# Performance work log

Measured on AMD Instinct MI355X. Metric: run time of the kernel, lower is better.

## Reference

```python
import jax, jax.numpy as jnp
import numpy as np

EPS = 1e-5
KS = 3
PAD = 1


def _bn(x, g, b, m, v):
    inv = g / jnp.sqrt(v + EPS)
    return x * inv[None, :, None, None] + (b - m * inv)[None, :, None, None]


def _deform_conv2d(x, off_w, off_b, w):
    # x: (B,C,H,W); off_w: (2*9,C,3,3); w: (Cout,C,3,3)
    B, C, H, W = x.shape
    N = KS * KS
    off = jax.lax.conv_general_dilated(x, off_w, (1, 1), ((PAD, PAD), (PAD, PAD)))
    off = off + off_b[None, :, None, None]                      # (B,2N,H,W)
    xp = jnp.pad(x, ((0, 0), (0, 0), (PAD, PAD), (PAD, PAD)))
    Hp, Wp = H + 2 * PAD, W + 2 * PAD
    r = jnp.arange(KS, dtype=x.dtype) - (KS - 1) // 2           # kernel offsets
    pny = jnp.repeat(r, KS)                                     # row-major (dy)
    pnx = jnp.tile(r, KS)                                       # row-major (dx)
    p0y = jnp.arange(1, H + 1, dtype=x.dtype)[None, None, :, None]
    p0x = jnp.arange(1, W + 1, dtype=x.dtype)[None, None, None, :]
    py = off[:, :N] + pny[None, :, None, None] + p0y            # (B,N,H,W)
    px = off[:, N:] + pnx[None, :, None, None] + p0x
    py = jnp.clip(py, 0.0, Hp - 1.0)
    px = jnp.clip(px, 0.0, Wp - 1.0)
    fy = jax.lax.stop_gradient(jnp.floor(py))                   # indices detached (as in torch impl)
    fx = jax.lax.stop_gradient(jnp.floor(px))
    qy0 = jnp.clip(fy, 0.0, Hp - 1.0)
    qx0 = jnp.clip(fx, 0.0, Wp - 1.0)
    qy1 = jnp.clip(fy + 1.0, 0.0, Hp - 1.0)
    qx1 = jnp.clip(fx + 1.0, 0.0, Wp - 1.0)
    xf = xp.reshape(B, C, Hp * Wp)

    def gather(qy, qx):
        idx = (qy * Wp + qx).astype(jnp.int32)                  # (B,N,H,W)
        return jax.vmap(lambda m_, i_: m_[:, i_])(xf, idx)       # (B,C,N,H,W)

    g_lt = (1.0 + (qy0 - py)) * (1.0 + (qx0 - px))
    g_rb = (1.0 - (qy1 - py)) * (1.0 - (qx1 - px))
    g_lb = (1.0 + (qy0 - py)) * (1.0 - (qx1 - px))
    g_rt = (1.0 - (qy1 - py)) * (1.0 + (qx0 - px))
    xo = (g_lt[:, None] * gather(qy0, qx0) + g_rb[:, None] * gather(qy1, qx1)
          + g_lb[:, None] * gather(qy0, qx1) + g_rt[:, None] * gather(qy1, qx0))
    # (B,C,N,H,W) -> (B,C,H*KS,W*KS): N = (row, col) row-major
    xo = xo.reshape(B, C, KS, KS, H, W).transpose(0, 1, 4, 2, 5, 3).reshape(B, C, H * KS, W * KS)
    return jax.lax.conv_general_dilated(xo, w, (KS, KS), 'VALID')


def _forward(x, dc1_offw, dc1_offb, dc1_w, bn1_g, bn1_b, bn1_m, bn1_v,
             dc2_offw, dc2_offb, dc2_w, bn2_g, bn2_b, bn2_m, bn2_v,
             id_w, id_b, bn3_g, bn3_b, bn3_m, bn3_v):
    h = jax.nn.relu(_bn(_deform_conv2d(x, dc1_offw, dc1_offb, dc1_w), bn1_g, bn1_b, bn1_m, bn1_v))
    h = _bn(_deform_conv2d(h, dc2_offw, dc2_offb, dc2_w), bn2_g, bn2_b, bn2_m, bn2_v)
    idt = jnp.einsum('bchw,oc->bohw', x, id_w[:, :, 0, 0]) + id_b[None, :, None, None]
    idt = _bn(idt, bn3_g, bn3_b, bn3_m, bn3_v)
    return jax.nn.relu(h + idt)


def setup_inputs() -> dict:
    key = jax.random.key(0)
    ks = jax.random.split(key, 16)
    B, Cin, Cout, H, W = 2, 64, 128, 128, 128
    N2 = 2 * KS * KS
    d = {}
    d['x'] = jax.random.normal(ks[0], (B, Cin, H, W), jnp.float32)
    d['dc1_offw'] = jax.random.normal(ks[1], (N2, Cin, KS, KS), jnp.float32) * 0.01
    d['dc1_offb'] = jnp.zeros((N2,), jnp.float32)
    d['dc1_w'] = jax.random.normal(ks[2], (Cout, Cin, KS, KS), jnp.float32) * 0.05
    d['bn1_g'] = 1.0 + 0.1 * jax.random.normal(ks[3], (Cout,), jnp.float32)
    d['bn1_b'] = 0.1 * jax.random.normal(ks[4], (Cout,), jnp.float32)
    d['bn1_m'] = 0.1 * jax.random.normal(ks[5], (Cout,), jnp.float32)
    d['bn1_v'] = jnp.ones((Cout,), jnp.float32)
    d['dc2_offw'] = jax.random.normal(ks[6], (N2, Cout, KS, KS), jnp.float32) * 0.01
    d['dc2_offb'] = jnp.zeros((N2,), jnp.float32)
    d['dc2_w'] = jax.random.normal(ks[7], (Cout, Cout, KS, KS), jnp.float32) * 0.03
    d['bn2_g'] = 1.0 + 0.1 * jax.random.normal(ks[8], (Cout,), jnp.float32)
    d['bn2_b'] = 0.1 * jax.random.normal(ks[9], (Cout,), jnp.float32)
    d['bn2_m'] = 0.1 * jax.random.normal(ks[10], (Cout,), jnp.float32)
    d['bn2_v'] = jnp.ones((Cout,), jnp.float32)
    d['id_w'] = jax.random.normal(ks[11], (Cout, Cin, 1, 1), jnp.float32) * 0.1
    d['id_b'] = jnp.zeros((Cout,), jnp.float32)
    d['bn3_g'] = 1.0 + 0.1 * jax.random.normal(ks[12], (Cout,), jnp.float32)
    d['bn3_b'] = 0.1 * jax.random.normal(ks[13], (Cout,), jnp.float32)
    d['bn3_m'] = 0.1 * jax.random.normal(ks[14], (Cout,), jnp.float32)
    d['bn3_v'] = jnp.ones((Cout,), jnp.float32)
    return d


def reference(x, dc1_offw, dc1_offb, dc1_w, bn1_g, bn1_b, bn1_m, bn1_v,
              dc2_offw, dc2_offb, dc2_w, bn2_g, bn2_b, bn2_m, bn2_v,
              id_w, id_b, bn3_g, bn3_b, bn3_m, bn3_v):
    return _forward(x, dc1_offw, dc1_offb, dc1_w, bn1_g, bn1_b, bn1_m, bn1_v,
                    dc2_offw, dc2_offb, dc2_w, bn2_g, bn2_b, bn2_m, bn2_v,
                    id_w, id_b, bn3_g, bn3_b, bn3_m, bn3_v)
```

## Files before the change

### kernel.cpp

```cpp
#include <hip/hip_runtime.h>
#include <math.h>

#define HH 128
#define WW 128
#define HWSZ (HH * WW)
#define BB 2
#define COUT 128

typedef __bf16 bf16x8 __attribute__((ext_vector_type(8)));
typedef float f32x4 __attribute__((ext_vector_type(4)));
typedef short s16x8 __attribute__((ext_vector_type(8)));
typedef short s16x4 __attribute__((ext_vector_type(4)));
typedef unsigned short u16x4 __attribute__((ext_vector_type(4)));
typedef unsigned short u16x8 __attribute__((ext_vector_type(8)));

__device__ __forceinline__ short tobf(float f) {
  union { float f; unsigned u; } v; v.f = f;
  unsigned r = v.u + 0x7fffu + ((v.u >> 16) & 1u);
  return (short)(r >> 16);
}
__device__ __forceinline__ float asf(unsigned u) {
  union { unsigned u; float f; } v; v.u = u;
  return v.f;
}

__global__ __launch_bounds__(256) void prep_scale_kernel(
    const float* __restrict__ src, const float* __restrict__ g,
    const float* __restrict__ v, short* __restrict__ dst,
    int K, int dstStride, int dstOff, int remapCin) {
  int k = blockIdx.x * 256 + threadIdx.x;
  int o = blockIdx.y;
  if (k >= K) return;
  float inv = g[o] / sqrtf(v[o] + 1e-5f);
  int col = remapCin ? (k % 9) * remapCin + (k / 9) : k;
  dst[(size_t)o * dstStride + dstOff + col] = tobf(src[(size_t)o * K + k] * inv);
}

__global__ __launch_bounds__(256) void prep_off_kernel(const float* __restrict__ src,
                                                       short* __restrict__ dst,
                                                       int K, int Cin) {
  int k = blockIdx.x * 256 + threadIdx.x;
  int o = blockIdx.y;
  if (k >= K) return;
  int col = (k % 9) * Cin + (k / 9);
  dst[(size_t)o * K + col] = (o < 18) ? tobf(src[(size_t)o * K + k]) : (short)0;
}

__global__ __launch_bounds__(128) void prep_bias_kernel(
    const float* b1, const float* m1, const float* g1, const float* v1,
    const float* b2, const float* m2, const float* g2, const float* v2,
    const float* b3, const float* m3, const float* g3, const float* v3,
    const float* idb, float* cb1, float* cb2) {
  int o = threadIdx.x;
  float inv1 = g1[o] / sqrtf(v1[o] + 1e-5f);
  float inv2 = g2[o] / sqrtf(v2[o] + 1e-5f);
  float inv3 = g3[o] / sqrtf(v3[o] + 1e-5f);
  cb1[o] = b1[o] - m1[o] * inv1;
  cb2[o] = (b2[o] - m2[o] * inv2) + idb[o] * inv3 + (b3[o] - m3[o] * inv3);
}

__global__ __launch_bounds__(256) void xcast_kernel(const float* __restrict__ x,
                                                    unsigned short* __restrict__ xn) {
  __shared__ short lds[64 * 72];
  int tid = threadIdx.x;
  int gp0 = blockIdx.x * 64;
  int b = gp0 >> 14;
  int pl0 = gp0 & 16383;
  int p = tid & 63;
  int cb = (tid >> 6) * 16;
#pragma unroll
  for (int i = 0; i < 16; i++) {
    int c = cb + i;
    float v = x[((size_t)(b * 64 + c)) * HWSZ + pl0 + p];
    lds[p * 72 + c] = tobf(v);
  }
  __syncthreads();
  int pw = tid >> 2, cseg = (tid & 3) * 16;
  u16x8 a = *(const u16x8*)&lds[pw * 72 + cseg];
  u16x8 b8 = *(const u16x8*)&lds[pw * 72 + cseg + 8];
  *(u16x8*)&xn[(size_t)(gp0 + pw) * 64 + cseg] = a;
  *(u16x8*)&xn[(size_t)(gp0 + pw) * 64 + cseg + 8] = b8;
}

__global__ __launch_bounds__(512, 4) void offconv_mfma_kernel(
    const unsigned short* __restrict__ in, const short* __restrict__ woff,
    const float* __restrict__ offb, float* __restrict__ off, int cshift) {
  __shared__ short wlds[32 * 40];
  __shared__ short vlds[64 * 40];
  const int tid = threadIdx.x;
  const int lane = tid & 63;
  const int wv = tid >> 6;
  const int pb = ((blockIdx.x & 7) << 6) | (blockIdx.x >> 3);
  const int pix0 = pb << 6;
  const int x0 = pix0 & 127, y = (pix0 >> 7) & 127, b = pix0 >> 14;
  const int Cin = 1 << cshift;
  const int Kc = 9 << cshift;
  const unsigned short* inb = in + (size_t)b * HWSZ * Cin;
  const int ps = tid >> 3, cq = tid & 7;
  const int l15 = lane & 15, quad = lane >> 4;
  const int ptile = wv & 3, otile = wv >> 2;

  f32x4 acc = {0.f, 0.f, 0.f, 0.f};

  for (int k0 = 0; k0 < Kc; k0 += 32) {
    s16x8 wreg;
    if (tid < 128) wreg = *(const s16x8*)&woff[(size_t)(tid >> 2) * Kc + k0 + (tid & 3) * 8];
    int n = k0 >> cshift;
    int dy = n / 3 - 1, dx = n % 3 - 1;
    int yy = y + dy;
    int xx = x0 + ps + dx;
    int c0 = (k0 & (Cin - 1)) + cq * 4;
    u16x4 pk = {0, 0, 0, 0};
    if (((unsigned)yy < (unsigned)HH) && ((unsigned)xx < (unsigned)WW))
      pk = *(const u16x4*)&inb[((size_t)yy * WW + xx) * Cin + c0];
    __syncthreads();
    if (tid < 128) *(s16x8*)&wlds[(tid >> 2) * 40 + (tid & 3) * 8] = wreg;
    *(u16x4*)&vlds[ps * 40 + cq * 4] = pk;
    __syncthreads();
    bf16x8 bfr = *(const bf16x8*)&vlds[(ptile * 16 + l15) * 40 + quad * 8];
    bf16x8 afr = *(const bf16x8*)&wlds[(otile * 16 + l15) * 40 + quad * 8];
    acc = __builtin_amdgcn_mfma_f32_16x16x32_bf16(afr, bfr, acc, 0, 0, 0);
  }
#pragma unroll
  for (int r = 0; r < 4; r++) {
    int o = otile * 16 + quad * 4 + r;
    if (o < 18)
      off[(size_t)(b * 18 + o) * HWSZ + y * WW + x0 + ptile * 16 + l15] = acc[r] + offb[o];
  }
}

__global__ __launch_bounds__(512, 4) void deform_mfma_kernel(
    const unsigned short* __restrict__ in, const float* __restrict__ off,
    const short* __restrict__ wbf, const float* __restrict__ cbv,
    const unsigned short* __restrict__ xid, float* __restrict__ outf,
    unsigned short* __restrict__ outb, int cshift, int KCONV, int KTOT, int mode) {
  __shared__ __align__(16) char smem[33792];
  float4* dw = (float4*)smem;
  int4* da = (int4*)(smem + 9216);
  short* wlds = (short*)(smem + 18432);
  short* vlds = (short*)(smem + 28672);
  short* trans = (short*)smem;

  const int tid = threadIdx.x;
  const int lane = tid & 63;
  const int wv = tid >> 6;
  const int pb = ((blockIdx.x & 7) << 6) | (blockIdx.x >> 3);
  const int pix0 = pb << 6;
  const int x0 = pix0 & 127, y = (pix0 >> 7) & 127, b = pix0 >> 14;
  const int Cin = 1 << cshift;
  const unsigned short* inb = in + (size_t)b * HWSZ * Cin;
  const int ps = tid >> 3, cq = tid & 7;
  const int l15 = lane & 15, quad = lane >> 4;
  const int ptile = wv & 3, ohalf = wv >> 2;

  for (int t = tid; t < 576; t += 512) {
    int n = t >> 6, pp = t & 63;
    float offy = off[(size_t)(b * 18 + n) * HWSZ + y * WW + x0 + pp];
    float offx = off[(size_t)(b * 18 + 9 + n) * HWSZ + y * WW + x0 + pp];
    float py = offy + (float)(n / 3 - 1) + (float)(y + 1);
    float px = offx + (float)(n % 3 - 1) + (float)(x0 + pp + 1);
    py = fminf(fmaxf(py, 0.f), 129.f);
    px = fminf(fmaxf(px, 0.f), 129.f);
    float fy = floorf(py), fx = floorf(px);
    float qy1 = fminf(fy + 1.f, 129.f), qx1 = fminf(fx + 1.f, 129.f);
    float ty0 = 1.f + fy - py, ty1 = 1.f - (qy1 - py);
    float tx0 = 1.f + fx - px, tx1 = 1.f - (qx1 - px);
    int iy0 = (int)fy - 1, ix0 = (int)fx - 1;
    int iy1 = (int)qy1 - 1, ix1 = (int)qx1 - 1;
    if ((unsigned)iy0 >= (unsigned)HH) ty0 = 0.f;
    if ((unsigned)iy1 >= (unsigned)HH) ty1 = 0.f;
    if ((unsigned)ix0 >= (unsigned)WW) tx0 = 0.f;
    if ((unsigned)ix1 >= (unsigned)WW) tx1 = 0.f;
    int by0 = min(max(iy0, 0), HH - 1), by1 = min(max(iy1, 0), HH - 1);
    int bx0 = min(max(ix0, 0), WW - 1), bx1 = min(max(ix1, 0), WW - 1);
    dw[t] = make_float4(ty0 * tx0, ty0 * tx1, ty1 * tx0, ty1 * tx1);
    da[t] = make_int4((by0 * WW + bx0) * Cin, (bx1 - bx0) * Cin,
                      (by1 - by0) * WW * Cin, 0);
  }

  f32x4 acc[4];
#pragma unroll
  for (int i = 0; i < 4; i++) acc[i] = (f32x4){0.f, 0.f, 0.f, 0.f};
  __syncthreads();

  for (int k0 = 0; k0 < KTOT; k0 += 32) {
    s16x8 wreg = *(const s16x8*)&wbf[(size_t)(tid >> 2) * KTOT + k0 + (tid & 3) * 8];
    u16x4 pk;
    if (k0 < KCONV) {
      int n = k0 >> cshift;
      int c0 = (k0 & (Cin - 1)) + cq * 4;
      int d = n * 64 + ps;
      float4 w = dw[d];
      int4 a = da[d];
      const unsigned short* ptr = inb + a.x + c0;
      uint2 t00 = *(const uint2*)(ptr);
      uint2 t01 = *(const uint2*)(ptr + a.y);
      uint2 t10 = *(const uint2*)(ptr + a.z);
      uint2 t11 = *(const uint2*)(ptr + a.y + a.z);
      float v0 = w.x * asf(t00.x << 16) + w.y * asf(t01.x << 16)
               + w.z * asf(t10.x << 16) + w.w * asf(t11.x << 16);
      float v1 = w.x * asf(t00.x & 0xffff0000u) + w.y * asf(t01.x & 0xffff0000u)
               + w.z * asf(t10.x & 0xffff0000u) + w.w * asf(t11.x & 0xffff0000u);
      float v2 = w.x * asf(t00.y << 16) + w.y * asf(t01.y << 16)
               + w.z * asf(t10.y << 16) + w.w * asf(t11.y << 16);
      float v3 = w.x * asf(t00.y & 0xffff0000u) + w.y * asf(t01.y & 0xffff0000u)
               + w.z * asf(t10.y & 0xffff0000u) + w.w * asf(t11.y & 0xffff0000u);
      pk[0] = (unsigned short)tobf(v0);
      pk[1] = (unsigned short)tobf(v1);
      pk[2] = (unsigned short)tobf(v2);
      pk[3] = (unsigned short)tobf(v3);
    } else {
      int c = k0 - KCONV + cq * 4;
      pk = *(const u16x4*)&xid[((size_t)(b * HWSZ) + y * WW + x0 + ps) * 64 + c];
    }
    __syncthreads();
    *(s16x8*)&wlds[(tid >> 2) * 40 + (tid & 3) * 8] = wreg;
    *(u16x4*)&vlds[ps * 40 + cq * 4] = pk;
    __syncthreads();
    bf16x8 bfr = *(const bf16x8*)&vlds[(ptile * 16 + l15) * 40 + quad * 8];
#pragma unroll
    for (int ot = 0; ot < 4; ot++) {
      bf16x8 afr = *(const bf16x8*)&wlds[(ohalf * 64 + ot * 16 + l15) * 40 + quad * 8];
      acc[ot] = __builtin_amdgcn_mfma_f32_16x16x32_bf16(afr, bfr, acc[ot], 0, 0, 0);
    }
    __syncthreads();
  }

  if (mode == 1) {
    int px_ = x0 + ptile * 16 + l15;
#pragma unroll
    for (int ot = 0; ot < 4; ot++) {
#pragma unroll
      for (int r = 0; r < 4; r++) {
        int o = ohalf * 64 + ot * 16 + quad * 4 + r;
        float v = fmaxf(acc[ot][r] + cbv[o], 0.f);
        outf[(size_t)(b * COUT + o) * HWSZ + y * WW + px_] = v;
      }
    }
  } else {
    int pl = ptile * 16 + l15;
#pragma unroll
    for (int ot = 0; ot < 4; ot++) {
      s16x4 t4;
#pragma unroll
      for (int r = 0; r < 4; r++) {
        int o = ohalf * 64 + ot * 16 + quad * 4 + r;
        t4[r] = tobf(fmaxf(acc[ot][r] + cbv[o], 0.f));
      }
      *(s16x4*)&trans[pl * 136 + ohalf * 64 + ot * 16 + quad * 4] = t4;
    }
    __syncthreads();
    int pw = tid >> 3, cseg = (tid & 7) * 16;
    u16x8 a = *(const u16x8*)&trans[pw * 136 + cseg];
    u16x8 b8 = *(const u16x8*)&trans[pw * 136 + cseg + 8];
    size_t gb = ((size_t)(b * HWSZ) + y * WW + x0 + pw) * 128 + cseg;
    *(u16x8*)&outb[gb] = a;
    *(u16x8*)&outb[gb + 8] = b8;
  }
}

extern "C" void kernel_launch(void* const* d_in, const int* in_sizes, int n_in,
                              void* d_out, int out_size, void* d_ws, size_t ws_size,
                              hipStream_t stream) {
  const float* x        = (const float*)d_in[0];
  const float* dc1_offw = (const float*)d_in[1];
  const float* dc1_offb = (const float*)d_in[2];
  const float* dc1_w    = (const float*)d_in[3];
  const float* bn1_g    = (const float*)d_in[4];
  const float* bn1_b    = (const float*)d_in[5];
  const float* bn1_m    = (const float*)d_in[6];
  const float* bn1_v    = (const float*)d_in[7];
  const float* dc2_offw = (const float*)d_in[8];
  const float* dc2_offb = (const float*)d_in[9];
  const float* dc2_w    = (const float*)d_in[10];
  const float* bn2_g    = (const float*)d_in[11];
  const float* bn2_b    = (const float*)d_in[12];
  const float* bn2_m    = (const float*)d_in[13];
  const float* bn2_v    = (const float*)d_in[14];
  const float* id_w     = (const float*)d_in[15];
  const float* id_b     = (const float*)d_in[16];
  const float* bn3_g    = (const float*)d_in[17];
  const float* bn3_b    = (const float*)d_in[18];
  const float* bn3_m    = (const float*)d_in[19];
  const float* bn3_v    = (const float*)d_in[20];

  float* wsf = (float*)d_ws;
  float* off1 = wsf;
  float* off2 = off1 + (size_t)BB * 18 * HWSZ;
  float* cb1  = off2 + (size_t)BB * 18 * HWSZ;
  float* cb2  = cb1 + 128;
  unsigned short* xbf = (unsigned short*)(cb2 + 128);
  unsigned short* h1  = xbf + (size_t)BB * HWSZ * 64;
  short* wbf1  = (short*)(h1 + (size_t)BB * HWSZ * COUT);
  short* wbf2  = wbf1 + (size_t)128 * 576;
  short* woff1 = wbf2 + (size_t)128 * 1216;
  short* woff2 = woff1 + (size_t)32 * 576;

  const int K1 = 576, K2 = 1152, KT2 = 1216;

  hipLaunchKernelGGL(prep_scale_kernel, dim3((K1 + 255) / 256, 128), dim3(256), 0, stream,
                     dc1_w, bn1_g, bn1_v, wbf1, K1, K1, 0, 64);
  hipLaunchKernelGGL(prep_scale_kernel, dim3((K2 + 255) / 256, 128), dim3(256), 0, stream,
                     dc2_w, bn2_g, bn2_v, wbf2, K2, KT2, 0, 128);
  hipLaunchKernelGGL(prep_scale_kernel, dim3(1, 128), dim3(256), 0, stream,
                     id_w, bn3_g, bn3_v, wbf2, 64, KT2, K2, 0);
  hipLaunchKernelGGL(prep_off_kernel, dim3((K1 + 255) / 256, 32), dim3(256), 0, stream,
                     dc1_offw, woff1, K1, 64);
  hipLaunchKernelGGL(prep_off_kernel, dim3((K2 + 255) / 256, 32), dim3(256), 0, stream,
                     dc2_offw, woff2, K2, 128);
  hipLaunchKernelGGL(prep_bias_kernel, dim3(1), dim3(128), 0, stream,
                     bn1_b, bn1_m, bn1_g, bn1_v, bn2_b, bn2_m, bn2_g, bn2_v,
                     bn3_b, bn3_m, bn3_g, bn3_v, id_b, cb1, cb2);
  hipLaunchKernelGGL(xcast_kernel, dim3(BB * HWSZ / 64), dim3(256), 0, stream, x, xbf);

  hipLaunchKernelGGL(offconv_mfma_kernel, dim3(512), dim3(512), 0, stream,
                     xbf, woff1, dc1_offb, off1, 6);
  hipLaunchKernelGGL(deform_mfma_kernel, dim3(512), dim3(512), 0, stream,
                     xbf, off1, wbf1, cb1, (const unsigned short*)nullptr,
                     (float*)nullptr, h1, 6, K1, K1, 0);
  hipLaunchKernelGGL(offconv_mfma_kernel, dim3(512), dim3(512), 0, stream,
                     h1, woff2, dc2_offb, off2, 7);
  hipLaunchKernelGGL(deform_mfma_kernel, dim3(512), dim3(512), 0, stream,
                     h1, off2, wbf2, cb2, xbf, (float*)d_out,
                     (unsigned short*)nullptr, 7, K2, KT2, 1);
}
```

Baseline: 210.5 us.

## Double-buffer LDS in conv kernels, fuse prep kernels, retile offset conv

Both MFMA conv kernels now use double-buffered LDS: global loads for the next K-chunk are issued before the current chunk's MFMAs, and written to the alternate buffer afterwards. This leaves one barrier per iteration instead of two and hides load latency. The six weight/bias prep kernels are merged into one launch. The offset conv moves to 256-thread blocks of 32 pixels with twice as many blocks. The bilinear interpolation math is also vectorized with packed float2 ops. Costs are larger LDS use in the deform kernel (48KB), which may lower occupancy, and more live registers.

```diff
diff --git a/kernel.cpp b/kernel.cpp
--- a/kernel.cpp
+++ b/kernel.cpp
@@ -9,6 +9,7 @@
 
 typedef __bf16 bf16x8 __attribute__((ext_vector_type(8)));
 typedef float f32x4 __attribute__((ext_vector_type(4)));
+typedef float f32x2 __attribute__((ext_vector_type(2)));
 typedef short s16x8 __attribute__((ext_vector_type(8)));
 typedef short s16x4 __attribute__((ext_vector_type(4)));
 typedef unsigned short u16x4 __attribute__((ext_vector_type(4)));
@@ -23,40 +24,72 @@
   union { unsigned u; float f; } v; v.u = u;
   return v.f;
 }
-
-__global__ __launch_bounds__(256) void prep_scale_kernel(
-    const float* __restrict__ src, const float* __restrict__ g,
-    const float* __restrict__ v, short* __restrict__ dst,
-    int K, int dstStride, int dstOff, int remapCin) {
-  int k = blockIdx.x * 256 + threadIdx.x;
-  int o = blockIdx.y;
-  if (k >= K) return;
-  float inv = g[o] / sqrtf(v[o] + 1e-5f);
-  int col = remapCin ? (k % 9) * remapCin + (k / 9) : k;
-  dst[(size_t)o * dstStride + dstOff + col] = tobf(src[(size_t)o * K + k] * inv);
-}
-
-__global__ __launch_bounds__(256) void prep_off_kernel(const float* __restrict__ src,
-                                                       short* __restrict__ dst,
-                                                       int K, int Cin) {
-  int k = blockIdx.x * 256 + threadIdx.x;
-  int o = blockIdx.y;
-  if (k >= K) return;
-  int col = (k % 9) * Cin + (k / 9);
-  dst[(size_t)o * K + col] = (o < 18) ? tobf(src[(size_t)o * K + k]) : (short)0;
-}
-
-__global__ __launch_bounds__(128) void prep_bias_kernel(
-    const float* b1, const float* m1, const float* g1, const float* v1,
-    const float* b2, const float* m2, const float* g2, const float* v2,
-    const float* b3, const float* m3, const float* g3, const float* v3,
-    const float* idb, float* cb1, float* cb2) {
-  int o = threadIdx.x;
-  float inv1 = g1[o] / sqrtf(v1[o] + 1e-5f);
-  float inv2 = g2[o] / sqrtf(v2[o] + 1e-5f);
-  float inv3 = g3[o] / sqrtf(v3[o] + 1e-5f);
-  cb1[o] = b1[o] - m1[o] * inv1;
-  cb2[o] = (b2[o] - m2[o] * inv2) + idb[o] * inv3 + (b3[o] - m3[o] * inv3);
+__device__ __forceinline__ f32x2 up2(unsigned u) {
+  f32x2 r; r[0] = asf(u << 16); r[1] = asf(u & 0xffff0000u); return r;
+}
+__device__ __forceinline__ unsigned pack2bf(float a, float b) {
+  union { float f; unsigned u; } x, y; x.f = a; y.f = b;
+  unsigned lo = (x.u + 0x7fffu + ((x.u >> 16) & 1u)) >> 16;
+  unsigned hi = (y.u + 0x7fffu + ((y.u >> 16) & 1u)) & 0xffff0000u;
+  return lo | hi;
+}
+
+#define PA0 73728
+#define PA1 221184
+#define PA2 229376
+#define PA3 247808
+#define PA4 284672
+#define PA5 284928
+__global__ __launch_bounds__(256) void prep_all_kernel(
+    const float* __restrict__ dc1_w, const float* __restrict__ dc2_w,
+    const float* __restrict__ id_w, const float* __restrict__ dc1_offw,
+    const float* __restrict__ dc2_offw,
+    const float* g1, const float* b1, const float* m1, const float* v1,
+    const float* g2, const float* b2, const float* m2, const float* v2,
+    const float* g3, const float* b3, const float* m3, const float* v3,
+    const float* idb,
+    short* __restrict__ wbf1, short* __restrict__ wbf2,
+    short* __restrict__ woff1, short* __restrict__ woff2,
+    float* __restrict__ cb1, float* __restrict__ cb2) {
+  int idx = blockIdx.x * 256 + threadIdx.x;
+  if (idx < PA0) {
+    int o = idx / 576, k = idx - o * 576;
+    float inv = g1[o] / sqrtf(v1[o] + 1e-5f);
+    int col = (k % 9) * 64 + k / 9;
+    wbf1[o * 576 + col] = tobf(dc1_w[(size_t)o * 576 + k] * inv);
+  } else if (idx < PA1) {
+    int j = idx - PA0;
+    int o = j / 1152, k = j - o * 1152;
+    float inv = g2[o] / sqrtf(v2[o] + 1e-5f);
+    int col = (k % 9) * 128 + k / 9;
+    wbf2[o * 1216 + col] = tobf(dc2_w[(size_t)o * 1152 + k] * inv);
+  } else if (idx < PA2) {
+    int j = idx - PA1;
+    int o = j >> 6, k = j & 63;
+    float inv = g3[o] / sqrtf(v3[o] + 1e-5f);
+    wbf2[o * 1216 + 1152 + k] = tobf(id_w[(size_t)o * 64 + k] * inv);
+  } else if (idx < PA3) {
+    int j = idx - PA2;
+    int o = j / 576, k = j - o * 576;
+    int col = (k % 9) * 64 + k / 9;
+    woff1[o * 576 + col] = (o < 18) ? tobf(dc1_offw[(size_t)o * 576 + k]) : (short)0;
+  } else if (idx < PA4) {
+    int j = idx - PA3;
+    int o = j / 1152, k = j - o * 1152;
+    int col = (k % 9) * 128 + k / 9;
+    woff2[o * 1152 + col] = (o < 18) ? tobf(dc2_offw[(size_t)o * 1152 + k]) : (short)0;
+  } else if (idx < PA5) {
+    int j = idx - PA4;
+    if (j < 128) {
+      float inv = g1[j] / sqrtf(v1[j] + 1e-5f);
+      cb1[j] = b1[j] - m1[j] * inv;
+    } else {
+      int o = j - 128;
+      float inv2_ = g2[o] / sqrtf(v2[o] + 1e-5f);
+      float inv3_ = g3[o] / sqrtf(v3[o] + 1e-5f);
+      cb2[o] = (b2[o] - m2[o] * inv2_) + idb[o] * inv3_ + (b3[o] - m3[o] * inv3_);
+    }
+  }
 }
 
 __global__ __launch_bounds__(256) void xcast_kernel(const float* __restrict__ x,
@@ -71,8 +104,7 @@
 #pragma unroll
   for (int i = 0; i < 16; i++) {
     int c = cb + i;
-    float v = x[((size_t)(b * 64 + c)) * HWSZ + pl0 + p];
-    lds[p * 72 + c] = tobf(v);
+    lds[p * 72 + c] = tobf(x[((size_t)(b * 64 + c)) * HWSZ + pl0 + p]);
   }
   __syncthreads();
   int pw = tid >> 2, cseg = (tid & 3) * 16;
@@ -82,44 +114,55 @@
   *(u16x8*)&xn[(size_t)(gp0 + pw) * 64 + cseg + 8] = b8;
 }
 
-__global__ __launch_bounds__(512, 4) void offconv_mfma_kernel(
+__global__ __launch_bounds__(256, 8) void offconv_mfma_kernel(
     const unsigned short* __restrict__ in, const short* __restrict__ woff,
     const float* __restrict__ offb, float* __restrict__ off, int cshift) {
-  __shared__ short wlds[32 * 40];
-  __shared__ short vlds[64 * 40];
+  __shared__ short wlds[2][32 * 40];
+  __shared__ short vlds[2][32 * 40];
   const int tid = threadIdx.x;
-  const int lane = tid & 63;
-  const int wv = tid >> 6;
-  const int pb = ((blockIdx.x & 7) << 6) | (blockIdx.x >> 3);
-  const int pix0 = pb << 6;
+  const int lane = tid & 63, wv = tid >> 6;
+  const int pb = ((blockIdx.x & 7) << 7) | (blockIdx.x >> 3);
+  const int pix0 = pb << 5;
   const int x0 = pix0 & 127, y = (pix0 >> 7) & 127, b = pix0 >> 14;
   const int Cin = 1 << cshift;
   const int Kc = 9 << cshift;
   const unsigned short* inb = in + (size_t)b * HWSZ * Cin;
   const int ps = tid >> 3, cq = tid & 7;
   const int l15 = lane & 15, quad = lane >> 4;
-  const int ptile = wv & 3, otile = wv >> 2;
-
-  f32x4 acc = {0.f, 0.f, 0.f, 0.f};
-
-  for (int k0 = 0; k0 < Kc; k0 += 32) {
-    s16x8 wreg;
+  const int ptile = wv & 1, otile = wv >> 1;
+
+  s16x8 wreg;
+  u16x4 pk;
+  auto issue = [&](int k0) {
     if (tid < 128) wreg = *(const s16x8*)&woff[(size_t)(tid >> 2) * Kc + k0 + (tid & 3) * 8];
     int n = k0 >> cshift;
     int dy = n / 3 - 1, dx = n % 3 - 1;
     int yy = y + dy;
     int xx = x0 + ps + dx;
     int c0 = (k0 & (Cin - 1)) + cq * 4;
-    u16x4 pk = {0, 0, 0, 0};
+    pk = (u16x4){0, 0, 0, 0};
     if (((unsigned)yy < (unsigned)HH) && ((unsigned)xx < (unsigned)WW))
       pk = *(const u16x4*)&inb[((size_t)yy * WW + xx) * Cin + c0];
+  };
+  auto commit = [&](int buf) {
+    if (tid < 128) *(s16x8*)&wlds[buf][(tid >> 2) * 40 + (tid & 3) * 8] = wreg;
+    *(u16x4*)&vlds[buf][ps * 40 + cq * 4] = pk;
+  };
+
+  f32x4 acc = {0.f, 0.f, 0.f, 0.f};
+  issue(0);
+  commit(0);
+  __syncthreads();
+  const int NC = Kc >> 5;
+  for (int ch = 0; ch < NC; ch++) {
+    int cur = ch & 1;
+    bool has = (ch + 1) < NC;
+    if (has) issue((ch + 1) << 5);
+    bf16x8 bfr = *(const bf16x8*)&vlds[cur][(ptile * 16 + l15) * 40 + quad * 8];
+    bf16x8 afr = *(const bf16x8*)&wlds[cur][(otile * 16 + l15) * 40 + quad * 8];
+    acc = __builtin_amdgcn_mfma_f32_16x16x32_bf16(afr, bfr, acc, 0, 0, 0);
+    if (has) commit(cur ^ 1);
     __syncthreads();
-    if (tid < 128) *(s16x8*)&wlds[(tid >> 2) * 40 + (tid & 3) * 8] = wreg;
-    *(u16x4*)&vlds[ps * 40 + cq * 4] = pk;
-    __syncthreads();
-    bf16x8 bfr = *(const bf16x8*)&vlds[(ptile * 16 + l15) * 40 + quad * 8];
-    bf16x8 afr = *(const bf16x8*)&wlds[(otile * 16 + l15) * 40 + quad * 8];
-    acc = __builtin_amdgcn_mfma_f32_16x16x32_bf16(afr, bfr, acc, 0, 0, 0);
   }
 #pragma unroll
   for (int r = 0; r < 4; r++) {
@@ -134,16 +177,15 @@
     const short* __restrict__ wbf, const float* __restrict__ cbv,
     const unsigned short* __restrict__ xid, float* __restrict__ outf,
     unsigned short* __restrict__ outb, int cshift, int KCONV, int KTOT, int mode) {
-  __shared__ __align__(16) char smem[33792];
+  __shared__ __align__(16) char smem[49152];
   float4* dw = (float4*)smem;
   int4* da = (int4*)(smem + 9216);
   short* wlds = (short*)(smem + 18432);
-  short* vlds = (short*)(smem + 28672);
+  short* vlds = (short*)(smem + 38912);
   short* trans = (short*)smem;
 
   const int tid = threadIdx.x;
-  const int lane = tid & 63;
-  const int wv = tid >> 6;
+  const int lane = tid & 63, wv = tid >> 6;
   const int pb = ((blockIdx.x & 7) << 6) | (blockIdx.x >> 3);
   const int pix0 = pb << 6;
   const int x0 = pix0 & 127, y = (pix0 >> 7) & 127, b = pix0 >> 14;
@@ -151,7 +193,7 @@
   const unsigned short* inb = in + (size_t)b * HWSZ * Cin;
   const int ps = tid >> 3, cq = tid & 7;
   const int l15 = lane & 15, quad = lane >> 4;
-  const int ptile = wv & 3, ohalf = wv >> 2;
+  const int ptile = wv & 3, og = wv >> 2;
 
   for (int t = tid; t < 576; t += 512) {
     int n = t >> 6, pp = t & 63;
@@ -181,48 +223,64 @@
   f32x4 acc[4];
 #pragma unroll
   for (int i = 0; i < 4; i++) acc[i] = (f32x4){0.f, 0.f, 0.f, 0.f};
-  __syncthreads();
-
-  for (int k0 = 0; k0 < KTOT; k0 += 32) {
-    s16x8 wreg = *(const s16x8*)&wbf[(size_t)(tid >> 2) * KTOT + k0 + (tid & 3) * 8];
-    u16x4 pk;
+
+  s16x8 wreg;
+  uint2 t00, t01, t10, t11, pkr;
+  float4 wgt;
+  int isres = 0;
+
+  auto issue = [&](int k0) {
+    wreg = *(const s16x8*)&wbf[(size_t)(tid >> 2) * KTOT + k0 + (tid & 3) * 8];
     if (k0 < KCONV) {
+      isres = 0;
       int n = k0 >> cshift;
       int c0 = (k0 & (Cin - 1)) + cq * 4;
-      int d = n * 64 + ps;
-      float4 w = dw[d];
+      int d = (n << 6) + ps;
+      wgt = dw[d];
       int4 a = da[d];
       const unsigned short* ptr = inb + a.x + c0;
-      uint2 t00 = *(const uint2*)(ptr);
-      uint2 t01 = *(const uint2*)(ptr + a.y);
-      uint2 t10 = *(const uint2*)(ptr + a.z);
-      uint2 t11 = *(const uint2*)(ptr + a.y + a.z);
-      float v0 = w.x * asf(t00.x << 16) + w.y * asf(t01.x << 16)
-               + w.z * asf(t10.x << 16) + w.w * asf(t11.x << 16);
-      float v1 = w.x * asf(t00.x & 0xffff0000u) + w.y * asf(t01.x & 0xffff0000u)
-               + w.z * asf(t10.x & 0xffff0000u) + w.w * asf(t11.x & 0xffff0000u);
-      float v2 = w.x * asf(t00.y << 16) + w.y * asf(t01.y << 16)
-               + w.z * asf(t10.y << 16) + w.w * asf(t11.y << 16);
-      float v3 = w.x * asf(t00.y & 0xffff0000u) + w.y * asf(t01.y & 0xffff0000u)
-               + w.z * asf(t10.y & 0xffff0000u) + w.w * asf(t11.y & 0xffff0000u);
-      pk[0] = (unsigned short)tobf(v0);
-      pk[1] = (unsigned short)tobf(v1);
-      pk[2] = (unsigned short)tobf(v2);
-      pk[3] = (unsigned short)tobf(v3);
+      t00 = *(const uint2*)(ptr);
+      t01 = *(const uint2*)(ptr + a.y);
+      t10 = *(const uint2*)(ptr + a.z);
+      t11 = *(const uint2*)(ptr + a.y + a.z);
     } else {
+      isres = 1;
       int c = k0 - KCONV + cq * 4;
-      pk = *(const u16x4*)&xid[((size_t)(b * HWSZ) + y * WW + x0 + ps) * 64 + c];
-    }
-    __syncthreads();
-    *(s16x8*)&wlds[(tid >> 2) * 40 + (tid & 3) * 8] = wreg;
-    *(u16x4*)&vlds[ps * 40 + cq * 4] = pk;
-    __syncthreads();
-    bf16x8 bfr = *(const bf16x8*)&vlds[(ptile * 16 + l15) * 40 + quad * 8];
+      pkr = *(const uint2*)&xid[((size_t)(b * HWSZ) + y * WW + x0 + ps) * 64 + c];
+    }
+  };
+  auto commit = [&](int buf) {
+    uint2 pk;
+    if (!isres) {
+      f32x2 v0 = up2(t00.x) * wgt.x + up2(t01.x) * wgt.y
+               + up2(t10.x) * wgt.z + up2(t11.x) * wgt.w;
+      f32x2 v1 = up2(t00.y) * wgt.x + up2(t01.y) * wgt.y
+               + up2(t10.y) * wgt.z + up2(t11.y) * wgt.w;
+      pk.x = pack2bf(v0[0], v0[1]);
+      pk.y = pack2bf(v1[0], v1[1]);
+    } else {
+      pk = pkr;
+    }
+    *(s16x8*)&wlds[buf * 5120 + (tid >> 2) * 40 + (tid & 3) * 8] = wreg;
+    *(uint2*)&vlds[buf * 2560 + ps * 40 + cq * 4] = pk;
+  };
+
+  __syncthreads();
+  issue(0);
+  commit(0);
+  __syncthreads();
+  const int NC = KTOT >> 5;
+  for (int ch = 0; ch < NC; ch++) {
+    int cur = ch & 1;
+    bool has = (ch + 1) < NC;
+    if (has) issue((ch + 1) << 5);
+    bf16x8 bfr = *(const bf16x8*)&vlds[cur * 2560 + (ptile * 16 + l15) * 40 + quad * 8];
 #pragma unroll
     for (int ot = 0; ot < 4; ot++) {
-      bf16x8 afr = *(const bf16x8*)&wlds[(ohalf * 64 + ot * 16 + l15) * 40 + quad * 8];
+      bf16x8 afr = *(const bf16x8*)&wlds[cur * 5120 + (og * 64 + ot * 16 + l15) * 40 + quad * 8];
       acc[ot] = __builtin_amdgcn_mfma_f32_16x16x32_bf16(afr, bfr, acc[ot], 0, 0, 0);
     }
+    if (has) commit(cur ^ 1);
     __syncthreads();
   }
 
@@ -232,9 +290,9 @@
     for (int ot = 0; ot < 4; ot++) {
 #pragma unroll
       for (int r = 0; r < 4; r++) {
-        int o = ohalf * 64 + ot * 16 + quad * 4 + r;
-        float v = fmaxf(acc[ot][r] + cbv[o], 0.f);
-        outf[(size_t)(b * COUT + o) * HWSZ + y * WW + px_] = v;
+        int o = og * 64 + ot * 16 + quad * 4 + r;
+        outf[(size_t)(b * COUT + o) * HWSZ + y * WW + px_] =
+            fmaxf(acc[ot][r] + cbv[o], 0.f);
       }
     }
   } else {
@@ -244,10 +302,10 @@
       s16x4 t4;
 #pragma unroll
       for (int r = 0; r < 4; r++) {
-        int o = ohalf * 64 + ot * 16 + quad * 4 + r;
+        int o = og * 64 + ot * 16 + quad * 4 + r;
         t4[r] = tobf(fmaxf(acc[ot][r] + cbv[o], 0.f));
       }
-      *(s16x4*)&trans[pl * 136 + ohalf * 64 + ot * 16 + quad * 4] = t4;
+      *(s16x4*)&trans[pl * 136 + og * 64 + ot * 16 + quad * 4] = t4;
     }
     __syncthreads();
     int pw = tid >> 3, cseg = (tid & 7) * 16;
@@ -298,27 +356,19 @@
 
   const int K1 = 576, K2 = 1152, KT2 = 1216;
 
-  hipLaunchKernelGGL(prep_scale_kernel, dim3((K1 + 255) / 256, 128), dim3(256), 0, stream,
-                     dc1_w, bn1_g, bn1_v, wbf1, K1, K1, 0, 64);
-  hipLaunchKernelGGL(prep_scale_kernel, dim3((K2 + 255) / 256, 128), dim3(256), 0, stream,
-                     dc2_w, bn2_g, bn2_v, wbf2, K2, KT2, 0, 128);
-  hipLaunchKernelGGL(prep_scale_kernel, dim3(1, 128), dim3(256), 0, stream,
-                     id_w, bn3_g, bn3_v, wbf2, 64, KT2, K2, 0);
-  hipLaunchKernelGGL(prep_off_kernel, dim3((K1 + 255) / 256, 32), dim3(256), 0, stream,
-                     dc1_offw, woff1, K1, 64);
-  hipLaunchKernelGGL(prep_off_kernel, dim3((K2 + 255) / 256, 32), dim3(256), 0, stream,
-                     dc2_offw, woff2, K2, 128);
-  hipLaunchKernelGGL(prep_bias_kernel, dim3(1), dim3(128), 0, stream,
-                     bn1_b, bn1_m, bn1_g, bn1_v, bn2_b, bn2_m, bn2_g, bn2_v,
-                     bn3_b, bn3_m, bn3_g, bn3_v, id_b, cb1, cb2);
+  hipLaunchKernelGGL(prep_all_kernel, dim3((PA5 + 255) / 256), dim3(256), 0, stream,
+                     dc1_w, dc2_w, id_w, dc1_offw, dc2_offw,
+                     bn1_g, bn1_b, bn1_m, bn1_v, bn2_g, bn2_b, bn2_m, bn2_v,
+                     bn3_g, bn3_b, bn3_m, bn3_v, id_b,
+                     wbf1, wbf2, woff1, woff2, cb1, cb2);
   hipLaunchKernelGGL(xcast_kernel, dim3(BB * HWSZ / 64), dim3(256), 0, stream, x, xbf);
 
-  hipLaunchKernelGGL(offconv_mfma_kernel, dim3(512), dim3(512), 0, stream,
+  hipLaunchKernelGGL(offconv_mfma_kernel, dim3(1024), dim3(256), 0, stream,
                      xbf, woff1, dc1_offb, off1, 6);
   hipLaunchKernelGGL(deform_mfma_kernel, dim3(512), dim3(512), 0, stream,
                      xbf, off1, wbf1, cb1, (const unsigned short*)nullptr,
                      (float*)nullptr, h1, 6, K1, K1, 0);
-  hipLaunchKernelGGL(offconv_mfma_kernel, dim3(512), dim3(512), 0, stream,
+  hipLaunchKernelGGL(offconv_mfma_kernel, dim3(1024), dim3(256), 0, stream,
                      h1, woff2, dc2_offb, off2, 7);
   hipLaunchKernelGGL(deform_mfma_kernel, dim3(512), dim3(512), 0, stream,
                      h1, off2, wbf2, cb2, xbf, (float*)d_out,
```

Measured after the change: 195.7 us. -7.0%, faster.
